# Kernel tuning notes

Measured on AMD Instinct MI355X. Metric: run time of the kernel, lower is better.

The kernel has to match this reference:

```python
import jax, jax.numpy as jnp
import numpy as np
import math

EPS = jnp.float32(1.1920929e-07)      # torch.finfo(torch.float).eps
FMIN = jnp.finfo(jnp.float32).min     # torch.finfo(torch.float).min
NEG = jnp.float32(-1e9)


def setup_inputs() -> dict:
    key = jax.random.key(0)
    ks = jax.random.split(key, 9)
    bs, l, sub, tgt, hidden, t_vocab, voc = 16, 1024, 2, 256, 512, 2000, 3000
    return {
        "out_logits": jax.random.normal(ks[0], (bs, tgt, t_vocab), jnp.float32),
        "feature": jax.random.normal(ks[1], (bs, tgt, hidden), jnp.float32),
        "memory_raw": jax.random.normal(ks[2], (bs, l, hidden), jnp.float32),
        "content_e": jax.random.randint(ks[3], (bs, l * sub), 0, voc, jnp.int64
                                        if jax.config.jax_enable_x64 else jnp.int32),
        "Wq": jax.random.normal(ks[4], (hidden, hidden), jnp.float32) * 0.02,
        "bq": jax.random.normal(ks[5], (hidden,), jnp.float32) * 0.02,
        "Wk": jax.random.normal(ks[6], (hidden, hidden * sub), jnp.float32) * 0.02,
        "bk": jax.random.normal(ks[7], (hidden * sub,), jnp.float32) * 0.02,
        "sentinel": jax.random.uniform(ks[8], (1, hidden), jnp.float32),
        "voc_len": 3000,
    }


def reference(out_logits, feature, memory_raw, content_e, Wq, bq, Wk, bk, sentinel, voc_len):
    bs, l, hidden = memory_raw.shape
    tgt_len = feature.shape[1]
    subtokens = Wk.shape[1] // hidden
    src_len = l * subtokens

    # decode(): out = log_softmax(prob(feature)); key_linear + subtoken expansion
    out = jax.nn.log_softmax(out_logits, axis=-1)                     # (bs, t, t_vocab)
    memory = (memory_raw @ Wk + bk).reshape(bs, src_len, hidden)      # (bs, s, h)
    key_padding_mask = content_e == 0                                 # (bs, s)

    # pointer(): attention over memory + sentinel
    pointer_key = jnp.concatenate(
        [memory, jnp.broadcast_to(sentinel[None, :, :], (bs, 1, hidden))], axis=1)
    pointer_query = jax.nn.gelu(feature @ Wq + bq, approximate=False) # (bs, t, h)
    atten = jnp.einsum('bth,bsh->bts', pointer_query, pointer_key) / math.sqrt(hidden)

    mask = jnp.concatenate(
        [key_padding_mask, jnp.zeros((bs, 1), bool)], axis=-1)[:, None, :]
    atten = jnp.where(mask, NEG, atten)
    atten = jax.nn.log_softmax(atten, axis=-1)                        # (bs, t, s+1)

    pointer_gate = atten[:, :, -1:]                                   # (bs, t, 1)
    exp_atten = jnp.exp(atten[:, :, :-1])                             # (bs, t, s)

    # scatter-add over src positions by extended-vocab id (== one-hot M einsum)
    def scat(ea_b, ce_b):  # ea_b: (t, s)  ce_b: (s,)
        return jax.ops.segment_sum(ea_b.T, ce_b, num_segments=voc_len).T  # (t, voc)
    pointer_atten_p = jax.vmap(scat)(exp_atten, content_e)            # (bs, t, voc)

    pointer_atten_log = jnp.log(pointer_atten_p + EPS)
    pointer_atten_log = pointer_atten_log - jnp.log1p(-jnp.exp(pointer_gate) + EPS)
    pointer_atten_log = jnp.where(jnp.isneginf(pointer_atten_log), FMIN, pointer_atten_log)

    pad = jnp.full((bs, tgt_len, voc_len - out.shape[-1]), -jnp.inf, jnp.float32)
    out = jnp.concatenate([out, pad], axis=-1)                        # (bs, t, voc)

    p = jnp.stack([out + pointer_gate,
                   pointer_atten_log + jnp.log(1.0 - jnp.exp(pointer_gate) + EPS)],
                  axis=-2)                                            # (bs, t, 2, voc)
    return jax.scipy.special.logsumexp(p, axis=-2)                    # (bs, t, voc)
```

## Files before the change

### kernel.cpp

```cpp
#include <hip/hip_runtime.h>
#include <math.h>

#define BSZ   16
#define LSEQ  1024
#define TGT   256
#define HID   512
#define TV    2000
#define VOC   3000
#define SRC   2048
#define NKE   1280
#define JOFF  640
#define SCALE 0.044194173824159216f

typedef unsigned short u16;
typedef __attribute__((ext_vector_type(8))) short bf16x8;
typedef __attribute__((ext_vector_type(4))) float f32x4;

__device__ __forceinline__ u16 f2bf(float x) {
    unsigned u = __float_as_uint(x);
    u += 0x7FFFu + ((u >> 16) & 1u);
    return (u16)(u >> 16);
}
__device__ __forceinline__ float bf2f(u16 x) {
    return __uint_as_float((unsigned)x << 16);
}

static __device__ __forceinline__ float gelu_exact(float x) {
    return 0.5f * x * (1.0f + erff(x * 0.70710678118654752f));
}

__device__ __forceinline__ void gload16(const u16* g, u16* l) {
    __builtin_amdgcn_global_load_lds(
        (const __attribute__((address_space(1))) unsigned int*)g,
        (__attribute__((address_space(3))) unsigned int*)l,
        16, 0, 0);
}

__device__ __forceinline__ void cast8_body(const float4* __restrict__ in,
                                           int4* __restrict__ out, int i) {
    float4 x = in[2 * i], y = in[2 * i + 1];
    unsigned p0 = (unsigned)f2bf(x.x) | ((unsigned)f2bf(x.y) << 16);
    unsigned p1 = (unsigned)f2bf(x.z) | ((unsigned)f2bf(x.w) << 16);
    unsigned p2 = (unsigned)f2bf(y.x) | ((unsigned)f2bf(y.y) << 16);
    unsigned p3 = (unsigned)f2bf(y.z) | ((unsigned)f2bf(y.w) << 16);
    out[i] = make_int4(p0, p1, p2, p3);
}

__global__ __launch_bounds__(256) void prep(
    const float* __restrict__ memory_raw, const float* __restrict__ feature,
    const float* __restrict__ Wq, const float* __restrict__ Wk,
    const float* __restrict__ sentinel, const float* __restrict__ bk,
    const float* __restrict__ logits, const int* __restrict__ ce,
    int4* __restrict__ memb, int4* __restrict__ featb,
    u16* __restrict__ wqT, u16* __restrict__ wkE,
    float* __restrict__ rowsum, float* __restrict__ lse,
    int* __restrict__ boff, u16* __restrict__ bucket)
{
    __shared__ float t[32][33];
    __shared__ int cnt[VOC];
    __shared__ int part[256];
    const int id = blockIdx.x;
    const int tid = threadIdx.x;
    if (id < 4096) {
        cast8_body((const float4*)memory_raw, memb, id * 256 + tid);
    } else if (id < 5120) {
        cast8_body((const float4*)feature, featb, (id - 4096) * 256 + tid);
    } else if (id < 5376) {
        int id2 = id - 5120;
        int bx = (id2 & 15) * 32, by = (id2 >> 4) * 32;
        const int tx = tid & 31, ty = tid >> 5;
        #pragma unroll
        for (int k = 0; k < 4; ++k)
            t[ty + 8 * k][tx] = Wq[(size_t)(by + ty + 8 * k) * 512 + bx + tx];
        __syncthreads();
        #pragma unroll
        for (int k = 0; k < 4; ++k)
            wqT[(size_t)(bx + ty + 8 * k) * 512 + by + tx] = f2bf(t[tx][ty + 8 * k]);
    } else if (id < 5696) {
        const int rr = (id - 5376) * 4 + (tid >> 6);
        const int c = (tid & 63) * 8;
        const int j = rr >= JOFF;
        const int dd = rr - j * JOFF;
        u16* dst = wkE + (size_t)rr * HID + c;
        if (dd < 512) {
            const float* src = Wk + (size_t)dd * 1024 + j * 512 + c;
            #pragma unroll
            for (int k = 0; k < 8; ++k) dst[k] = f2bf(src[k]);
        } else if (dd == 512) {
            #pragma unroll
            for (int k = 0; k < 8; ++k) dst[k] = f2bf(sentinel[c + k]);
        } else if (dd == 513) {
            #pragma unroll
            for (int k = 0; k < 8; ++k) dst[k] = f2bf(bk[j * 512 + c + k]);
        } else {
            #pragma unroll
            for (int k = 0; k < 8; ++k) dst[k] = 0;
        }
    } else if (id == 5696) {
        float4* rz = (float4*)rowsum;
        for (int i = tid; i < 1024; i += 256) rz[i] = make_float4(0.f, 0.f, 0.f, 0.f);
    } else if (id < 6721) {
        const int row = (id - 5697) * 4 + (tid >> 6);
        const int lane = tid & 63;
        const float4* lrow4 = (const float4*)(logits + (size_t)row * TV);
        float4 v4[8];
        float m = -INFINITY;
        #pragma unroll
        for (int k = 0; k < 8; ++k) {
            int idx = lane + 64 * k;
            if (idx < 500) {
                v4[k] = lrow4[idx];
                m = fmaxf(m, fmaxf(fmaxf(v4[k].x, v4[k].y), fmaxf(v4[k].z, v4[k].w)));
            } else {
                v4[k] = make_float4(-INFINITY, -INFINITY, -INFINITY, -INFINITY);
            }
        }
        #pragma unroll
        for (int o = 32; o > 0; o >>= 1) m = fmaxf(m, __shfl_xor(m, o, 64));
        float s = 0.f;
        #pragma unroll
        for (int k = 0; k < 8; ++k)
            s += __expf(v4[k].x - m) + __expf(v4[k].y - m)
               + __expf(v4[k].z - m) + __expf(v4[k].w - m);
        #pragma unroll
        for (int o = 32; o > 0; o >>= 1) s += __shfl_xor(s, o, 64);
        if (lane == 0) lse[row] = m + __logf(s);
    } else {
        const int b = id - 6721;
        const int* ceb = ce + (size_t)b * SRC;
        for (int v = tid; v < VOC; v += 256) cnt[v] = 0;
        __syncthreads();
        for (int s = tid; s < SRC; s += 256) atomicAdd(&cnt[ceb[s]], 1);
        __syncthreads();
        const int base = tid * 12;
        int lc[12];
        int tot = 0;
        #pragma unroll
        for (int k = 0; k < 12; ++k) {
            int v = base + k;
            lc[k] = (v < VOC) ? cnt[v] : 0;
            tot += lc[k];
        }
        part[tid] = tot;
        __syncthreads();
        for (int d = 1; d < 256; d <<= 1) {
            int val = (tid >= d) ? part[tid - d] : 0;
            __syncthreads();
            part[tid] += val;
            __syncthreads();
        }
        int run = part[tid] - tot;
        int* boffb = boff + b * 3008;
        #pragma unroll
        for (int k = 0; k < 12; ++k) {
            int v = base + k;
            if (v < VOC) { boffb[v] = run; cnt[v] = run; run += lc[k]; }
        }
        if (tid == 0) boffb[VOC] = SRC;
        __syncthreads();
        for (int s = tid; s < SRC; s += 256) {
            int idv = ceb[s];
            int jl = (s & 1) * 1024 + (s >> 1);
            int pos = atomicAdd(&cnt[idv], 1);
            bucket[(size_t)b * SRC + pos] = (u16)jl;
        }
    }
}

__global__ __launch_bounds__(256) void gemm_query(
    const u16* __restrict__ feat, const u16* __restrict__ wqT,
    const float* __restrict__ bq, u16* __restrict__ queryb)
{
    __shared__ u16 As[2 * 2048];
    __shared__ u16 Bs[2 * 2048];
    const int tid = threadIdx.x;
    const int lane = tid & 63;
    const int w = tid >> 6;
    const int wr = (w >> 1) * 32, wc = (w & 1) * 32;
    const int m0 = blockIdx.y * 64, n0 = blockIdx.x * 64;

    const int srow = tid >> 2, scol = (tid & 3) * 8;
    const u16* gA = feat + (size_t)(m0 + srow) * HID + scol;
    const u16* gB = wqT + (size_t)(n0 + srow) * HID + scol;

    const int la = lane & 15, lb = lane >> 4;
    f32x4 acc[2][2] = {};

    gload16(gA, As + w * 512);
    gload16(gB, Bs + w * 512);

    int cur = 0;
    for (int k0 = 0; k0 < HID; k0 += 32) {
        __syncthreads();
        const u16* Asb = As + cur * 2048;
        const u16* Bsb = Bs + cur * 2048;
        bf16x8 af[2], bf[2];
        #pragma unroll
        for (int i = 0; i < 2; ++i)
            af[i] = *(const bf16x8*)(Asb + (wr + i * 16 + la) * 32 + lb * 8);
        #pragma unroll
        for (int j = 0; j < 2; ++j)
            bf[j] = *(const bf16x8*)(Bsb + (wc + j * 16 + la) * 32 + lb * 8);
        if (k0 + 32 < HID) {
            const int nb = cur ^ 1;
            gload16(gA + k0 + 32, As + nb * 2048 + w * 512);
            gload16(gB + k0 + 32, Bs + nb * 2048 + w * 512);
        }
        #pragma unroll
        for (int i = 0; i < 2; ++i)
            #pragma unroll
            for (int j = 0; j < 2; ++j)
                acc[i][j] = __builtin_amdgcn_mfma_f32_16x16x32_bf16(af[i], bf[j], acc[i][j], 0, 0, 0);
        cur ^= 1;
    }

    const int r_l = (lane >> 4) * 4, c_l = lane & 15;
    #pragma unroll
    for (int j = 0; j < 2; ++j) {
        const int n = n0 + wc + j * 16 + c_l;
        const float bv = bq[n];
        #pragma unroll
        for (int i = 0; i < 2; ++i)
            #pragma unroll
            for (int r = 0; r < 4; ++r) {
                const int m = m0 + wr + i * 16 + r_l + r;
                queryb[(size_t)m * HID + n] = f2bf(gelu_exact(acc[i][j][r] + bv));
            }
    }
}

template<int EPI, int LDA, int LDB>
__device__ __forceinline__ void gemm_body(
    int m0, int n0, int z,
    const u16* __restrict__ Abase, const u16* __restrict__ Bbase,
    u16* __restrict__ outb,
    const int* __restrict__ ce, float* __restrict__ rowsum,
    u16* __restrict__ As, u16* __restrict__ Bs)
{
    const int tid = threadIdx.x;
    const int lane = tid & 63;
    const int w = tid >> 6;
    const int wr = (w >> 1) * 64, wc = (w & 1) * 64;

    const u16* Ag = Abase;
    const u16* Bg = Bbase;
    if (EPI == 2) {
        Ag = Abase + (size_t)(z >> 1) * LSEQ * HID;
        Bg = Bbase + (size_t)(z >> 1) * TGT * NKE + (size_t)(z & 1) * JOFF;
    }

    const int chunkrow = lane >> 2;
    const int colc = (lane & 3) * 8;
    const int c0 = w * 2, c1 = c0 + 1;
    const u16* gA0 = Ag + (size_t)(m0 + c0 * 16 + chunkrow) * LDA + colc;
    const u16* gA1 = Ag + (size_t)(m0 + c1 * 16 + chunkrow) * LDA + colc;
    const u16* gB0 = Bg + (size_t)(n0 + c0 * 16 + chunkrow) * LDB + colc;
    const u16* gB1 = Bg + (size_t)(n0 + c1 * 16 + chunkrow) * LDB + colc;

    const int la = lane & 15, lb = lane >> 4;
    f32x4 acc[4][4] = {};

    gload16(gA0, As + c0 * 512);
    gload16(gA1, As + c1 * 512);
    gload16(gB0, Bs + c0 * 512);
    gload16(gB1, Bs + c1 * 512);

    int cur = 0;
    for (int k0 = 0; k0 < HID; k0 += 32) {
        __syncthreads();
        const u16* Asb = As + cur * 4096;
        const u16* Bsb = Bs + cur * 4096;
        bf16x8 af[4], bfv[4];
        #pragma unroll
        for (int i = 0; i < 4; ++i)
            af[i] = *(const bf16x8*)(Asb + (wr + i * 16 + la) * 32 + lb * 8);
        #pragma unroll
        for (int j = 0; j < 4; ++j)
            bfv[j] = *(const bf16x8*)(Bsb + (wc + j * 16 + la) * 32 + lb * 8);
        if (k0 + 32 < HID) {
            const int nb = cur ^ 1;
            u16* An = As + nb * 4096;
            u16* Bn = Bs + nb * 4096;
            gload16(gA0 + k0 + 32, An + c0 * 512);
            gload16(gA1 + k0 + 32, An + c1 * 512);
            gload16(gB0 + k0 + 32, Bn + c0 * 512);
            gload16(gB1 + k0 + 32, Bn + c1 * 512);
        }
        #pragma unroll
        for (int i = 0; i < 4; ++i)
            #pragma unroll
            for (int j = 0; j < 4; ++j)
                acc[i][j] = __builtin_amdgcn_mfma_f32_16x16x32_bf16(af[i], bfv[j], acc[i][j], 0, 0, 0);
        cur ^= 1;
    }

    const int r_l = (lane >> 4) * 4, c_l = lane & 15;
    if (EPI == 3) {
        #pragma unroll
        for (int j = 0; j < 4; ++j) {
            const int n = n0 + wc + j * 16 + c_l;
            #pragma unroll
            for (int i = 0; i < 4; ++i)
                #pragma unroll
                for (int r = 0; r < 4; ++r) {
                    const int m = m0 + wr + i * 16 + r_l + r;
                    outb[(size_t)m * NKE + n] = f2bf(acc[i][j][r]);
                }
        }
    } else {
        const int b = z >> 1, jj = z & 1;
        float biasc[4];
        #pragma unroll
        for (int j = 0; j < 4; ++j) {
            const int n = n0 + wc + j * 16 + c_l;
            biasc[j] = bf2f(Bbase[(size_t)(b * TGT + n) * NKE + jj * JOFF + 513]);
        }
        const int* ceb = ce + (size_t)b * SRC;
        float csum[4] = {0.f, 0.f, 0.f, 0.f};
        #pragma unroll
        for (int i = 0; i < 4; ++i)
            #pragma unroll
            for (int r = 0; r < 4; ++r) {
                const int m = m0 + wr + i * 16 + r_l + r;
                const int cm = ceb[2 * m + jj];
                const size_t rowbase = ((size_t)b * SRC + jj * 1024 + m) * TGT;
                #pragma unroll
                for (int j = 0; j < 4; ++j) {
                    float ev = (cm == 0) ? 0.f
                             : __expf((acc[i][j][r] + biasc[j]) * SCALE);
                    outb[rowbase + n0 + wc + j * 16 + c_l] = f2bf(ev);
                    csum[j] += ev;
                }
            }
        #pragma unroll
        for (int j = 0; j < 4; ++j) {
            csum[j] += __shfl_xor(csum[j], 16, 64);
            csum[j] += __shfl_xor(csum[j], 32, 64);
        }
        const int jsel = lane >> 4;
        float myv = (jsel == 0) ? csum[0] : (jsel == 1) ? csum[1]
                  : (jsel == 2) ? csum[2] : csum[3];
        atomicAdd(&rowsum[b * TGT + n0 + wc + jsel * 16 + c_l], myv);
    }
}

__global__ __launch_bounds__(256) void gemm_qk(
    const u16* __restrict__ queryb, const u16* __restrict__ wkE,
    u16* __restrict__ qkb)
{
    __shared__ u16 As[2 * 4096];
    __shared__ u16 Bs[2 * 4096];
    gemm_body<3, 512, 512>(blockIdx.y * 128, blockIdx.x * 128, 0,
                           queryb, wkE, qkb, nullptr, nullptr, As, Bs);
}

__global__ __launch_bounds__(256) void gemm_atten(
    const u16* __restrict__ memb, const u16* __restrict__ qkb,
    const int* __restrict__ ce, float* __restrict__ rowsum,
    u16* __restrict__ etb)
{
    __shared__ u16 As[2 * 4096];
    __shared__ u16 Bs[2 * 4096];
    const int i = blockIdx.x;
    const int xcd = i & 7, slot = i >> 3;
    const int bjj = xcd + 8 * (slot >> 4);
    const int inner = slot & 15;
    gemm_body<2, 512, NKE>((inner >> 1) * 128, (inner & 1) * 128, bjj,
                           memb, qkb, etb, ce, rowsum, As, Bs);
}

__global__ __launch_bounds__(256) void combine(
    const u16* __restrict__ etb, const u16* __restrict__ bucket,
    const int* __restrict__ boff, const u16* __restrict__ qkb,
    const float* __restrict__ rowsum, const float* __restrict__ lse,
    const float* __restrict__ out_logits, float* __restrict__ out)
{
    __shared__ float acc[8][256];
    __shared__ u16 sbuck[SRC];
    __shared__ float rcInv[8], rcGZ[8], rcEdl[8], rcDl[8];
    const int i = blockIdx.x;
    const int xcd = i & 7, slot = i >> 3;
    const int b = xcd + 8 * (slot / 384);
    const int inner = slot % 384;
    const int tc = inner / 12, vs = inner % 12;
    const int t0 = tc * 8;
    const int vbase = vs * 256;
    const int tid = threadIdx.x;
    const float EPSF = 1.1920929e-07f;

    if (tid < 8) {
        const int bt = b * TGT + t0 + tid;
        const float sent_v = bf2f(qkb[(size_t)bt * NKE + 512]) * SCALE;
        const float se = __expf(sent_v);
        const float sm = rowsum[bt] + se;
        const float inv = 1.0f / sm;
        const float g = sent_v - __logf(sm);
        const float eg = se * inv;
        const float dl = __logf(1.0f - eg + EPSF) - log1pf(-eg + EPSF);
        rcInv[tid] = inv;
        rcGZ[tid] = g - lse[bt];
        rcEdl[tid] = __expf(dl);
        rcDl[tid] = dl;
    }

    const int* boffb = boff + b * 3008;
    const u16* bukb = bucket + (size_t)b * SRC;
    const u16* etbb = etb + (size_t)b * SRC * TGT;

    const int vend = (vbase + 256 < VOC) ? vbase + 256 : VOC;
    const int e_lo = boffb[vbase];
    const int e_hi = boffb[vend];
    for (int e = e_lo + tid; e < e_hi; e += 256) sbuck[e - e_lo] = bukb[e];
    __syncthreads();

    {
        float a[8] = {0.f, 0.f, 0.f, 0.f, 0.f, 0.f, 0.f, 0.f};
        const int v = vbase + tid;
        if (v < VOC) {
            const int i0 = boffb[v] - e_lo;
            const int i1 = boffb[v + 1] - e_lo;
            for (int e = i0; e < i1; ++e) {
                const int s = sbuck[e];
                int4 u = *(const int4*)(etbb + (size_t)s * TGT + t0);
                a[0] += bf2f((u16)(u.x & 0xffff));
                a[1] += bf2f((u16)((unsigned)u.x >> 16));
                a[2] += bf2f((u16)(u.y & 0xffff));
                a[3] += bf2f((u16)((unsigned)u.y >> 16));
                a[4] += bf2f((u16)(u.z & 0xffff));
                a[5] += bf2f((u16)((unsigned)u.z >> 16));
                a[6] += bf2f((u16)(u.w & 0xffff));
                a[7] += bf2f((u16)((unsigned)u.w >> 16));
            }
        }
        #pragma unroll
        for (int k = 0; k < 8; ++k) acc[k][tid] = a[k];
    }
    __syncthreads();

    const int r = tid >> 5;
    const int vl0 = tid & 31;
    const int bt = b * TGT + t0 + r;
    const float inv = rcInv[r], gZ = rcGZ[r], edl = rcEdl[r], dlv = rcDl[r];
    const float* lrow = out_logits + (size_t)bt * TV;
    float* orow = out + (size_t)bt * VOC;
    #pragma unroll
    for (int kk = 0; kk < 8; ++kk) {
        const int vloc = vl0 + 32 * kk;
        const int v = vbase + vloc;
        if (v >= VOC) continue;
        float pv = acc[r][vloc] * inv + EPSF;
        float o;
        if (v < TV) o = __logf(__expf(lrow[v] + gZ) + pv * edl);
        else        o = __logf(pv) + dlv;
        orow[v] = o;
    }
}

extern "C" void kernel_launch(void* const* d_in, const int* in_sizes, int n_in,
                              void* d_out, int out_size, void* d_ws, size_t ws_size,
                              hipStream_t stream) {
    const float* out_logits = (const float*)d_in[0];
    const float* feature    = (const float*)d_in[1];
    const float* memory_raw = (const float*)d_in[2];
    const int*   content_e  = (const int*)d_in[3];
    const float* Wq = (const float*)d_in[4];
    const float* bq = (const float*)d_in[5];
    const float* Wk = (const float*)d_in[6];
    const float* bk = (const float*)d_in[7];
    const float* sentinel = (const float*)d_in[8];
    float* out = (float*)d_out;

    u16* memb   = (u16*)d_ws;
    u16* featb  = memb   + (size_t)16384 * 512;
    u16* wqT    = featb  + (size_t)4096 * 512;
    u16* wkE    = wqT    + (size_t)512 * 512;
    u16* queryb = wkE    + (size_t)NKE * 512;
    u16* qkb    = queryb + (size_t)4096 * 512;
    u16* etb    = qkb    + (size_t)4096 * NKE;
    float* rowsum = (float*)(etb + (size_t)BSZ * SRC * TGT);
    float* lse   = rowsum + 4096;
    int* boff = (int*)(lse + 4096);
    u16* bucket = (u16*)(boff + 16 * 3008);

    prep<<<6737, 256, 0, stream>>>(memory_raw, feature, Wq, Wk, sentinel, bk,
                                   out_logits, content_e,
                                   (int4*)memb, (int4*)featb, wqT, wkE,
                                   rowsum, lse, boff, bucket);
    gemm_query<<<dim3(8, 64), 256, 0, stream>>>(featb, wqT, bq, queryb);
    gemm_qk<<<dim3(10, 32), 256, 0, stream>>>(queryb, wkE, qkb);
    gemm_atten<<<512, 256, 0, stream>>>(memb, qkb, content_e, rowsum, etb);
    combine<<<6144, 256, 0, stream>>>(etb, bucket, boff, qkb,
                                      rowsum, lse, out_logits, out);
}
```

Before: 98.07 us.

## Redistribute independent prep work into later GEMM launches to overlap with small GEMMs

The monolithic prep kernel is split up. Only feature/Wq/Wk casting stays up front. The memory_raw bf16 cast is folded into the query GEMM launch as extra blocks, and the logits LSE and bucket-sort work become extra blocks of the QK GEMM launch. The aim is to fill idle CUs during the small, under-occupied GEMMs and shorten the critical path before them. The cost is larger shared memory per block in the merged kernels, which could lower occupancy, and heterogeneous blocks competing in the same launch.

```diff
diff --git a/kernel.cpp b/kernel.cpp
--- a/kernel.cpp
+++ b/kernel.cpp
@@ -46,27 +46,20 @@
     out[i] = make_int4(p0, p1, p2, p3);
 }
 
-__global__ __launch_bounds__(256) void prep(
-    const float* __restrict__ memory_raw, const float* __restrict__ feature,
-    const float* __restrict__ Wq, const float* __restrict__ Wk,
-    const float* __restrict__ sentinel, const float* __restrict__ bk,
-    const float* __restrict__ logits, const int* __restrict__ ce,
-    int4* __restrict__ memb, int4* __restrict__ featb,
-    u16* __restrict__ wqT, u16* __restrict__ wkE,
-    float* __restrict__ rowsum, float* __restrict__ lse,
-    int* __restrict__ boff, u16* __restrict__ bucket)
+__global__ __launch_bounds__(256) void prep_a(
+    const float* __restrict__ feature, const float* __restrict__ Wq,
+    const float* __restrict__ Wk, const float* __restrict__ sentinel,
+    const float* __restrict__ bk,
+    int4* __restrict__ featb, u16* __restrict__ wqT, u16* __restrict__ wkE,
+    float* __restrict__ rowsum)
 {
     __shared__ float t[32][33];
-    __shared__ int cnt[VOC];
-    __shared__ int part[256];
     const int id = blockIdx.x;
     const int tid = threadIdx.x;
-    if (id < 4096) {
-        cast8_body((const float4*)memory_raw, memb, id * 256 + tid);
-    } else if (id < 5120) {
-        cast8_body((const float4*)feature, featb, (id - 4096) * 256 + tid);
-    } else if (id < 5376) {
-        int id2 = id - 5120;
+    if (id < 1024) {
+        cast8_body((const float4*)feature, featb, id * 256 + tid);
+    } else if (id < 1280) {
+        int id2 = id - 1024;
         int bx = (id2 & 15) * 32, by = (id2 >> 4) * 32;
         const int tx = tid & 31, ty = tid >> 5;
         #pragma unroll
@@ -76,8 +69,8 @@
         #pragma unroll
         for (int k = 0; k < 4; ++k)
             wqT[(size_t)(bx + ty + 8 * k) * 512 + by + tx] = f2bf(t[tx][ty + 8 * k]);
-    } else if (id < 5696) {
-        const int rr = (id - 5376) * 4 + (tid >> 6);
+    } else if (id < 1600) {
+        const int rr = (id - 1280) * 4 + (tid >> 6);
         const int c = (tid & 63) * 8;
         const int j = rr >= JOFF;
         const int dd = rr - j * JOFF;
@@ -96,88 +89,30 @@
             #pragma unroll
             for (int k = 0; k < 8; ++k) dst[k] = 0;
         }
-    } else if (id == 5696) {
+    } else {
         float4* rz = (float4*)rowsum;
         for (int i = tid; i < 1024; i += 256) rz[i] = make_float4(0.f, 0.f, 0.f, 0.f);
-    } else if (id < 6721) {
-        const int row = (id - 5697) * 4 + (tid >> 6);
-        const int lane = tid & 63;
-        const float4* lrow4 = (const float4*)(logits + (size_t)row * TV);
-        float4 v4[8];
-        float m = -INFINITY;
-        #pragma unroll
-        for (int k = 0; k < 8; ++k) {
-            int idx = lane + 64 * k;
-            if (idx < 500) {
-                v4[k] = lrow4[idx];
-                m = fmaxf(m, fmaxf(fmaxf(v4[k].x, v4[k].y), fmaxf(v4[k].z, v4[k].w)));
-            } else {
-                v4[k] = make_float4(-INFINITY, -INFINITY, -INFINITY, -INFINITY);
-            }
-        }
-        #pragma unroll
-        for (int o = 32; o > 0; o >>= 1) m = fmaxf(m, __shfl_xor(m, o, 64));
-        float s = 0.f;
-        #pragma unroll
-        for (int k = 0; k < 8; ++k)
-            s += __expf(v4[k].x - m) + __expf(v4[k].y - m)
-               + __expf(v4[k].z - m) + __expf(v4[k].w - m);
-        #pragma unroll
-        for (int o = 32; o > 0; o >>= 1) s += __shfl_xor(s, o, 64);
-        if (lane == 0) lse[row] = m + __logf(s);
-    } else {
-        const int b = id - 6721;
-        const int* ceb = ce + (size_t)b * SRC;
-        for (int v = tid; v < VOC; v += 256) cnt[v] = 0;
-        __syncthreads();
-        for (int s = tid; s < SRC; s += 256) atomicAdd(&cnt[ceb[s]], 1);
-        __syncthreads();
-        const int base = tid * 12;
-        int lc[12];
-        int tot = 0;
-        #pragma unroll
-        for (int k = 0; k < 12; ++k) {
-            int v = base + k;
-            lc[k] = (v < VOC) ? cnt[v] : 0;
-            tot += lc[k];
-        }
-        part[tid] = tot;
-        __syncthreads();
-        for (int d = 1; d < 256; d <<= 1) {
-            int val = (tid >= d) ? part[tid - d] : 0;
-            __syncthreads();
-            part[tid] += val;
-            __syncthreads();
-        }
-        int run = part[tid] - tot;
-        int* boffb = boff + b * 3008;
-        #pragma unroll
-        for (int k = 0; k < 12; ++k) {
-            int v = base + k;
-            if (v < VOC) { boffb[v] = run; cnt[v] = run; run += lc[k]; }
-        }
-        if (tid == 0) boffb[VOC] = SRC;
-        __syncthreads();
-        for (int s = tid; s < SRC; s += 256) {
-            int idv = ceb[s];
-            int jl = (s & 1) * 1024 + (s >> 1);
-            int pos = atomicAdd(&cnt[idv], 1);
-            bucket[(size_t)b * SRC + pos] = (u16)jl;
-        }
-    }
-}
-
-__global__ __launch_bounds__(256) void gemm_query(
+    }
+}
+
+__global__ __launch_bounds__(256) void k_query(
     const u16* __restrict__ feat, const u16* __restrict__ wqT,
-    const float* __restrict__ bq, u16* __restrict__ queryb)
+    const float* __restrict__ bq, u16* __restrict__ queryb,
+    const float* __restrict__ memory_raw, int4* __restrict__ memb)
 {
-    __shared__ u16 As[2 * 2048];
-    __shared__ u16 Bs[2 * 2048];
+    __shared__ u16 sbuf[2 * 2048 * 2];
+    const int id = blockIdx.x;
     const int tid = threadIdx.x;
+    if (id >= 512) {
+        cast8_body((const float4*)memory_raw, memb, (id - 512) * 256 + tid);
+        return;
+    }
+    u16* As = sbuf;
+    u16* Bs = sbuf + 2 * 2048;
     const int lane = tid & 63;
     const int w = tid >> 6;
     const int wr = (w >> 1) * 32, wc = (w & 1) * 32;
-    const int m0 = blockIdx.y * 64, n0 = blockIdx.x * 64;
+    const int m0 = (id >> 3) * 64, n0 = (id & 7) * 64;
 
     const int srow = tid >> 2, scol = (tid & 3) * 8;
     const u16* gA = feat + (size_t)(m0 + srow) * HID + scol;
@@ -344,14 +279,87 @@
     }
 }
 
-__global__ __launch_bounds__(256) void gemm_qk(
+__global__ __launch_bounds__(256) void k_qk(
     const u16* __restrict__ queryb, const u16* __restrict__ wkE,
-    u16* __restrict__ qkb)
+    u16* __restrict__ qkb,
+    const float* __restrict__ logits, float* __restrict__ lse,
+    const int* __restrict__ ce, int* __restrict__ boff, u16* __restrict__ bucket)
 {
-    __shared__ u16 As[2 * 4096];
-    __shared__ u16 Bs[2 * 4096];
-    gemm_body<3, 512, 512>(blockIdx.y * 128, blockIdx.x * 128, 0,
-                           queryb, wkE, qkb, nullptr, nullptr, As, Bs);
+    __shared__ u16 sbuf[4 * 4096];
+    const int id = blockIdx.x;
+    const int tid = threadIdx.x;
+    if (id < 320) {
+        gemm_body<3, 512, 512>((id / 10) * 128, (id % 10) * 128, 0,
+                               queryb, wkE, qkb, nullptr, nullptr,
+                               sbuf, sbuf + 2 * 4096);
+    } else if (id < 1344) {
+        const int row = (id - 320) * 4 + (tid >> 6);
+        const int lane = tid & 63;
+        const float4* lrow4 = (const float4*)(logits + (size_t)row * TV);
+        float4 v4[8];
+        float m = -INFINITY;
+        #pragma unroll
+        for (int k = 0; k < 8; ++k) {
+            int idx = lane + 64 * k;
+            if (idx < 500) {
+                v4[k] = lrow4[idx];
+                m = fmaxf(m, fmaxf(fmaxf(v4[k].x, v4[k].y), fmaxf(v4[k].z, v4[k].w)));
+            } else {
+                v4[k] = make_float4(-INFINITY, -INFINITY, -INFINITY, -INFINITY);
+            }
+        }
+        #pragma unroll
+        for (int o = 32; o > 0; o >>= 1) m = fmaxf(m, __shfl_xor(m, o, 64));
+        float s = 0.f;
+        #pragma unroll
+        for (int k = 0; k < 8; ++k)
+            s += __expf(v4[k].x - m) + __expf(v4[k].y - m)
+               + __expf(v4[k].z - m) + __expf(v4[k].w - m);
+        #pragma unroll
+        for (int o = 32; o > 0; o >>= 1) s += __shfl_xor(s, o, 64);
+        if (lane == 0) lse[row] = m + __logf(s);
+    } else {
+        const int b = id - 1344;
+        int* cnt = (int*)sbuf;
+        int* part = cnt + VOC;
+        const int* ceb = ce + (size_t)b * SRC;
+        for (int v = tid; v < VOC; v += 256) cnt[v] = 0;
+        __syncthreads();
+        for (int s = tid; s < SRC; s += 256) atomicAdd(&cnt[ceb[s]], 1);
+        __syncthreads();
+        const int base = tid * 12;
+        int lc[12];
+        int tot = 0;
+        #pragma unroll
+        for (int k = 0; k < 12; ++k) {
+            int v = base + k;
+            lc[k] = (v < VOC) ? cnt[v] : 0;
+            tot += lc[k];
+        }
+        part[tid] = tot;
+        __syncthreads();
+        for (int d = 1; d < 256; d <<= 1) {
+            int val = (tid >= d) ? part[tid - d] : 0;
+            __syncthreads();
+            part[tid] += val;
+            __syncthreads();
+        }
+        int run = part[tid] - tot;
+        int* boffb = boff + b * 3008;
+        #pragma unroll
+        for (int k = 0; k < 12; ++k) {
+            int v = base + k;
+            if (v < VOC) { boffb[v] = run; cnt[v] = run; run += lc[k]; }
+        }
+        if (tid == 0) boffb[VOC] = SRC;
+        __syncthreads();
+        for (int s = tid; s < SRC; s += 256) {
+            int idv = ceb[s];
+            int jl = (s & 1) * 1024 + (s >> 1);
+            int pos = atomicAdd(&cnt[idv], 1);
+            bucket[(size_t)b * SRC + pos] = (u16)jl;
+        }
+    }
 }
 
 __global__ __launch_bounds__(256) void gemm_atten(
@@ -482,12 +490,11 @@
     int* boff = (int*)(lse + 4096);
     u16* bucket = (u16*)(boff + 16 * 3008);
 
-    prep<<<6737, 256, 0, stream>>>(memory_raw, feature, Wq, Wk, sentinel, bk,
-                                   out_logits, content_e,
-                                   (int4*)memb, (int4*)featb, wqT, wkE,
-                                   rowsum, lse, boff, bucket);
-    gemm_query<<<dim3(8, 64), 256, 0, stream>>>(featb, wqT, bq, queryb);
-    gemm_qk<<<dim3(10, 32), 256, 0, stream>>>(queryb, wkE, qkb);
+    prep_a<<<1601, 256, 0, stream>>>(feature, Wq, Wk, sentinel, bk,
+                                     (int4*)featb, wqT, wkE, rowsum);
+    k_query<<<4608, 256, 0, stream>>>(featb, wqT, bq, queryb, memory_raw, (int4*)memb);
+    k_qk<<<1360, 256, 0, stream>>>(queryb, wkE, qkb, out_logits, lse,
+                                   content_e, boff, bucket);
     gemm_atten<<<512, 256, 0, stream>>>(memb, qkb, content_e, rowsum, etb);
     combine<<<6144, 256, 0, stream>>>(etb, bucket, boff, qkb,
                                       rowsum, lse, out_logits, out);
```

Result: faster. 93.32 us (-4.8%).
